# Performance work log

Measured on AMD Instinct MI355X. Metric: run time of the kernel, lower is better.

## Reference

```python
import jax, jax.numpy as jnp
import numpy as np
import math

B = 1; SEQ = 2048; CHUNK = 16; K = SEQ // CHUNK
DIM = 1024; NH = 16; HD = DIM // NH
NL = 2; NLF = 2; HID = 4096; VOCAB = 32000; CSP_MAX = 4
EPS = 1e-5
BS = CHUNK + 2                 # per-chunk decoder block: [fx, sep, tokens]
L = K * BS + 2                 # + trailing [fx_last, sep]


def rope_cache(n_pos, n_elem, base=10000.0):
    theta = 1.0 / (base ** (jnp.arange(0, n_elem, 2, dtype=jnp.float32) / n_elem))
    idx = jnp.outer(jnp.arange(n_pos, dtype=jnp.float32), theta)  # [n_pos, n_elem/2]
    cos = jnp.concatenate([jnp.cos(idx), jnp.cos(idx)], -1)
    sin = jnp.concatenate([jnp.sin(idx), jnp.sin(idx)], -1)
    return cos, sin  # [n_pos, n_elem]


def apply_rope(x, cos, sin):
    # x: [b, h, l, d]; cos/sin: [l, d] (rope_n_elem == head_dim)
    h = x.shape[-1] // 2
    rot = jnp.concatenate([-x[..., h:], x[..., :h]], -1)
    return x * cos + rot * sin


def rmsnorm(x, w):
    return x * jax.lax.rsqrt(jnp.mean(x * x, -1, keepdims=True) + EPS) * w


def attention(x, wqkv, wo, cos, sin, mask):
    b, l, d = x.shape
    qkv = (x @ wqkv).reshape(b, l, 3, NH, HD).transpose(2, 0, 3, 1, 4)
    q, k, v = qkv[0], qkv[1], qkv[2]            # [b, h, l, hd]
    q = apply_rope(q, cos, sin)
    k = apply_rope(k, cos, sin)
    s = jnp.einsum('bhqd,bhkd->bhqk', q, k) / math.sqrt(HD)
    if mask is not None:
        s = jnp.where(mask, s, jnp.float32(-1e30))
    o = jnp.einsum('bhqk,bhkd->bhqd', jax.nn.softmax(s, -1), v)
    return o.transpose(0, 2, 1, 3).reshape(b, l, d) @ wo


def block(x, ln1, wqkv, wo, ln2, wg, wu, wd, cos, sin, mask):
    x = x + attention(rmsnorm(x, ln1), wqkv, wo, cos, sin, mask)
    h = rmsnorm(x, ln2)
    return x + (jax.nn.silu(h @ wg) * (h @ wu)) @ wd


def cat_mask(n, bs):
    # CAT mask: (kv divides block-start | same block) & causal
    q = jnp.arange(n)[:, None]
    kv = jnp.arange(n)[None, :]
    return ((kv % bs == 0) | (q // bs == kv // bs)) & (q >= kv)


def setup_inputs() -> dict:
    key = jax.random.key(0)
    ks = jax.random.split(key, 24)
    w = lambda k, s: jax.random.normal(k, s, jnp.float32) * 0.02
    return {
        'input_ids': jax.random.randint(ks[0], (B, SEQ), 0, VOCAB, dtype=jnp.int32),
        'chunk_size_power': 4,
        'f_wte': w(ks[1], (VOCAB, DIM)), 'f_pos': w(ks[2], (SEQ, DIM)),
        'f_adapt': w(ks[3], (CSP_MAX + 1, DIM)),
        'f_ln1': jnp.ones((NLF, DIM)), 'f_ln2': jnp.ones((NLF, DIM)),
        'f_wqkv': w(ks[4], (NLF, DIM, 3 * DIM)), 'f_wo': w(ks[5], (NLF, DIM, DIM)),
        'f_wg': w(ks[6], (NLF, DIM, HID)), 'f_wu': w(ks[7], (NLF, DIM, HID)),
        'f_wd': w(ks[8], (NLF, HID, DIM)),
        'f_norm': jnp.ones((DIM,)), 'f_proj': w(ks[9], (DIM, CHUNK * DIM)),
        'dummy_fx': w(ks[10], (CSP_MAX + 1, DIM)), 'wte': w(ks[11], (VOCAB, DIM)),
        'sep': w(ks[12], (1, DIM)),
        'd_ln1': jnp.ones((NL, DIM)), 'd_ln2': jnp.ones((NL, DIM)),
        'd_wqkv': w(ks[13], (NL, DIM, 3 * DIM)), 'd_wo': w(ks[14], (NL, DIM, DIM)),
        'd_wg': w(ks[15], (NL, DIM, HID)), 'd_wu': w(ks[16], (NL, DIM, HID)),
        'd_wd': w(ks[17], (NL, HID, DIM)),
        'd_norm': jnp.ones((DIM,)), 'w_out': w(ks[18], (VOCAB, DIM)),
    }


def reference(input_ids, chunk_size_power, f_wte, f_pos, f_adapt, f_ln1, f_ln2,
              f_wqkv, f_wo, f_wg, f_wu, f_wd, f_norm, f_proj, dummy_fx, wte, sep,
              d_ln1, d_ln2, d_wqkv, d_wo, d_wg, d_wu, d_wd, d_norm, w_out):
    csp = int(chunk_size_power)
    ids = input_ids.reshape(B, K, CHUNK)
    cosf, sinf = rope_cache(2 + CHUNK, HD)

    def compress(ids_c, chunk_idx):
        # ids_c: [B, CHUNK] (one chunk, vmapped over K)
        x = f_wte[ids_c]
        adaptive = jnp.broadcast_to(f_adapt[csp], (B, 1, DIM))
        pos_tok = jnp.broadcast_to(f_pos[chunk_idx], (B, 1, DIM))
        x = jnp.concatenate([adaptive, pos_tok, x], 1)  # [B, CHUNK+2, DIM]
        for i in range(NLF):
            x = block(x, f_ln1[i], f_wqkv[i], f_wo[i], f_ln2[i],
                      f_wg[i], f_wu[i], f_wd[i], cosf, sinf, None)
        x = rmsnorm(x, f_norm)[:, 2:, :].reshape(B, CHUNK * DIM)
        # chunk_size_power == log2(CHUNK): bilinear interpolate to same size == identity
        return x @ f_proj.T  # [B, DIM]

    fx = jax.vmap(compress, in_axes=(1, 0), out_axes=1)(ids, jnp.arange(K))  # [B, K, DIM]

    fx_last = fx[:, -1:, :]
    dummy = jnp.broadcast_to(dummy_fx[csp], (B, 1, DIM))
    fx_sh = jnp.concatenate([dummy, fx[:, :-1, :]], 1)[:, :, None, :]  # [B, K, 1, DIM]
    sep_t = jnp.broadcast_to(sep[0], (B, K, 1, DIM))
    emb = wte[ids]  # [B, K, CHUNK, DIM]
    x = jnp.concatenate([fx_sh, sep_t, emb], 2).reshape(B, K * BS, DIM)
    x = jnp.concatenate([x, fx_last, jnp.broadcast_to(sep[0], (B, 1, DIM))], 1)  # [B, L, DIM]

    # per-block repeating RoPE positions (cache built for len BS, tiled)
    pos = jnp.tile(jnp.arange(BS), K + 1)[:L]
    cosb, sinb = rope_cache(BS, HD)
    cosd, sind = cosb[pos], sinb[pos]
    mask = cat_mask(L, BS)

    for i in range(NL):
        x = block(x, d_ln1[i], d_wqkv[i], d_wo[i], d_ln2[i],
                  d_wg[i], d_wu[i], d_wd[i], cosd, sind, mask)
    x = rmsnorm(x, d_norm)
    return x @ w_out.T  # [B, L, VOCAB]
```

## Files before the change

### kernel.cpp

```cpp
#include <hip/hip_runtime.h>
#include <math.h>

#define L_DEC 2306
#define MPAD 2560
#define T_FINE 2304

typedef float f32x4 __attribute__((ext_vector_type(4)));
typedef __bf16 bf16x8 __attribute__((ext_vector_type(8)));
typedef unsigned short u16;
typedef unsigned short us4 __attribute__((ext_vector_type(4)));
typedef unsigned short us8 __attribute__((ext_vector_type(8)));

#define GLOAD16(g, l) __builtin_amdgcn_global_load_lds( \
    (const __attribute__((address_space(1))) unsigned int*)(g), \
    (__attribute__((address_space(3))) unsigned int*)(l), 16, 0, 0)

__device__ __forceinline__ u16 f2bf(float f) {
  unsigned u = __float_as_uint(f);
  u += 0x7fffu + ((u >> 16) & 1u);
  return (u16)(u >> 16);
}

__device__ __forceinline__ int fix_csp(const int* p) {
  int c = p[0];
  if ((unsigned)c <= 4u) return c;
  float f = __uint_as_float((unsigned)c);
  int c2 = (int)f;
  return ((unsigned)c2 <= 4u) ? c2 : 4;
}

__device__ __forceinline__ void xcd_map(int gx, int gy, int& bm, int& bn, int TS) {
  const int nwg = gx * gy;
  const int orig = blockIdx.y * gx + blockIdx.x;
  const int q8 = nwg >> 3, r8 = nwg & 7;
  const int xcd = orig & 7, idx8 = orig >> 3;
  const int wg = (xcd < r8 ? xcd * (q8 + 1) : r8 * (q8 + 1) + (xcd - r8) * q8) + idx8;
  bm = (wg / gx) * TS;
  bn = (wg % gx) * TS;
}

template<int EPI>
__global__ __launch_bounds__(512, 1) void k_gemm3(const u16* __restrict__ A,
                                                  const u16* __restrict__ B,
                                                  float* __restrict__ C,
                                                  int N, int K, int Mstore)
{
  extern __shared__ u16 lds[];
  const int tid = threadIdx.x;
  int bm, bn; xcd_map(gridDim.x, gridDim.y, bm, bn, 256);
  const int w = tid >> 6, lane = tid & 63;
  const int wm = (w >> 2) * 128, wn = (w & 3) * 64;
  const int lr = lane & 15, kh = lane >> 4;

#define STAGE3(buf, kt) do {                                                   \
    u16* lA = lds + (buf) * 32768;                                             \
    u16* lB = lA + 16384;                                                      \
    _Pragma("unroll")                                                          \
    for (int p = 0; p < 4; ++p) {                                              \
      int e = p * 512 + tid;                                                   \
      int row = e >> 3;                                                        \
      int kc = ((e & 7) ^ (row & 7)) * 8;    \
      GLOAD16(A + (size_t)(bm + row) * K + (size_t)(kt) * 64 + kc, lA + e * 8);\
      GLOAD16(B + (size_t)(bn + row) * K + (size_t)(kt) * 64 + kc, lB + e * 8);\
    }                                                                          \
  } while (0)

  f32x4 acc[8][4] = {};
  const int nt = K >> 6;
  STAGE3(0, 0);
  __syncthreads();
  int cur = 0;
  for (int t = 0; t < nt; ++t) {
    if (t + 1 < nt) STAGE3(cur ^ 1, t + 1);
    const u16* pA = lds + cur * 32768;
    const u16* pB = pA + 16384;
    const int xr = (lr & 7) << 3;
#pragma unroll
    for (int kt2 = 0; kt2 < 2; ++kt2) {
      bf16x8 af[8], bf[4];
#pragma unroll
      for (int m = 0; m < 8; ++m)
        af[m] = *(const bf16x8*)&pA[(wm + m * 16 + lr) * 64 + ((kt2 * 32 + kh * 8) ^ xr)];
#pragma unroll
      for (int n = 0; n < 4; ++n)
        bf[n] = *(const bf16x8*)&pB[(wn + n * 16 + lr) * 64 + ((kt2 * 32 + kh * 8) ^ xr)];
#pragma unroll
      for (int m = 0; m < 8; ++m)
#pragma unroll
        for (int n = 0; n < 4; ++n)
          acc[m][n] = __builtin_amdgcn_mfma_f32_16x16x32_bf16(af[m], bf[n], acc[m][n], 0, 0, 0);
    }
    __syncthreads();
    cur ^= 1;
  }
#undef STAGE3

#pragma unroll
  for (int m = 0; m < 8; ++m) {
    int gr0 = bm + wm + m * 16 + kh * 4;
#pragma unroll
    for (int n = 0; n < 4; ++n) {
      int gc = bn + wn + n * 16 + lr;
#pragma unroll
      for (int r = 0; r < 4; ++r) {
        int gr = gr0 + r;
        if (gr < Mstore) C[(size_t)gr * N + gc] = acc[m][n][r];
      }
    }
  }
}

template<int EPI>
__global__ __launch_bounds__(512, 1) void k_gemm2(const u16* __restrict__ A,
                                                  const u16* __restrict__ B,
                                                  float* __restrict__ C,
                                                  u16* __restrict__ Cb,
                                                  int N, int K, int Mstore)
{
  __shared__ u16 As[2][8192];
  __shared__ u16 Bs[2][8192];
  const int tid = threadIdx.x;
  int bm, bn; xcd_map(gridDim.x, gridDim.y, bm, bn, 256);
  const int w = tid >> 6, lane = tid & 63;
  const int wm = (w >> 2) * 128, wn = (w & 3) * 64;
  const int lr = lane & 15, kh = lane >> 4;
  const int r0 = tid >> 2;
  const int ksrc = 8 * ((tid & 3) ^ ((tid >> 3) & 3));
  const u16* ga = A + (size_t)(bm + r0) * K + ksrc;
  const u16* gb = B + (size_t)(bn + r0) * K + ksrc;
  const size_t rstep = (size_t)128 * K;
  const int cola = (kh * 8) ^ (((lr >> 1) & 3) << 3);

#define STAGE2(buf, kt) do {                                   \
    const u16* gA = ga + (size_t)(kt) * 32;                    \
    const u16* gB = gb + (size_t)(kt) * 32;                    \
    GLOAD16(gA,         &As[buf][tid * 8]);                    \
    GLOAD16(gA + rstep, &As[buf][tid * 8 + 4096]);             \
    GLOAD16(gB,         &Bs[buf][tid * 8]);                    \
    GLOAD16(gB + rstep, &Bs[buf][tid * 8 + 4096]);             \
  } while (0)

  f32x4 acc[8][4] = {};
  const int nt = K >> 5;
  STAGE2(0, 0);
  __syncthreads();
  int cur = 0;
  for (int t = 0; t < nt; ++t) {
    if (t + 1 < nt) STAGE2(cur ^ 1, t + 1);
    bf16x8 af[8], bf[4];
#pragma unroll
    for (int m = 0; m < 8; ++m)
      af[m] = *(const bf16x8*)&As[cur][(wm + m * 16 + lr) * 32 + cola];
#pragma unroll
    for (int n = 0; n < 4; ++n)
      bf[n] = *(const bf16x8*)&Bs[cur][(wn + n * 16 + lr) * 32 + cola];
#pragma unroll
    for (int m = 0; m < 8; ++m)
#pragma unroll
      for (int n = 0; n < 4; ++n)
        acc[m][n] = __builtin_amdgcn_mfma_f32_16x16x32_bf16(af[m], bf[n], acc[m][n], 0, 0, 0);
    __syncthreads();
    cur ^= 1;
  }
#undef STAGE2

#pragma unroll
  for (int m = 0; m < 8; ++m) {
    int gr0 = bm + wm + m * 16 + kh * 4;
#pragma unroll
    for (int n = 0; n < 4; ++n) {
      int gc = bn + wn + n * 16 + lr;
#pragma unroll
      for (int r = 0; r < 4; ++r) {
        int gr = gr0 + r;
        if (gr < Mstore) C[(size_t)gr * N + gc] = acc[m][n][r];
      }
    }
  }
}

template<int EPI>
__global__ __launch_bounds__(256) void k_gemm_bt(const u16* __restrict__ A,
                                                 const u16* __restrict__ B,
                                                 float* __restrict__ C,
                                                 u16* __restrict__ Cb,
                                                 int N, int K, int Mstore, int kchunk)
{
  __shared__ u16 As[4096];
  __shared__ u16 Bs[4096];
  const int tid = threadIdx.x;
  int bm, bn; xcd_map(gridDim.x, gridDim.y, bm, bn, 128);
  const int k0 = blockIdx.z * kchunk;
  const int w = tid >> 6, lane = tid & 63;
  const int wm = (w >> 1) * 64, wn = (w & 1) * 64;
  const int lr = lane & 15, kh = lane >> 4;
  const int r0 = tid >> 2;
  const int ksrc = 8 * ((tid & 3) ^ ((tid >> 3) & 3));
  const int cola = (kh * 8) ^ (((lr >> 1) & 3) << 3);

  const u16* ga = A + (size_t)(bm + r0) * K + k0 + ksrc;
  const u16* gb = B + (size_t)(bn + r0) * K + k0 + ksrc;
  u16* la = &As[tid * 8];
  u16* lb = &Bs[tid * 8];
  const size_t rstep = (size_t)64 * K;

  f32x4 acc[4][4] = {};
  for (int kk = 0; kk < kchunk; kk += 32) {
    GLOAD16(ga, la); GLOAD16(ga + rstep, la + 2048);
    GLOAD16(gb, lb); GLOAD16(gb + rstep, lb + 2048);
    ga += 32; gb += 32;
    __syncthreads();
    bf16x8 af[4], bfr[4];
#pragma unroll
    for (int m = 0; m < 4; ++m)
      af[m] = *(const bf16x8*)&As[(wm + m * 16 + lr) * 32 + cola];
#pragma unroll
    for (int n = 0; n < 4; ++n)
      bfr[n] = *(const bf16x8*)&Bs[(wn + n * 16 + lr) * 32 + cola];
#pragma unroll
    for (int m = 0; m < 4; ++m)
#pragma unroll
      for (int n = 0; n < 4; ++n)
        acc[m][n] = __builtin_amdgcn_mfma_f32_16x16x32_bf16(af[m], bfr[n], acc[m][n], 0, 0, 0);
    __syncthreads();
  }

  float* Cz = (EPI == 0) ? C + (size_t)blockIdx.z * Mstore * N : C;
  const int N2 = N >> 1;
#pragma unroll
  for (int m = 0; m < 4; ++m) {
    int gr0 = bm + wm + m * 16 + kh * 4;
#pragma unroll
    for (int n = 0; n < 4; ++n) {
      int gc = bn + wn + n * 16 + lr;
#pragma unroll
      for (int r = 0; r < 4; ++r) {
        int gr = gr0 + r;
        if (EPI == 2) {
          float x = acc[m][n][r];
          float px = __shfl_xor(x, 1);
          if (!(lr & 1) && gr < Mstore) {
            float s = x / (1.f + expf(-x)) * px;
            Cb[(size_t)gr * N2 + (gc >> 1)] = f2bf(s);
          }
        } else if (gr < Mstore) {
          size_t off = (size_t)gr * N + gc;
          if (EPI == 0) Cz[off] = acc[m][n][r];
          else          C[off] += acc[m][n][r];
        }
      }
    }
  }
}

__global__ __launch_bounds__(256) void k_gemm_hf(const u16* __restrict__ A,
                                                 const float* __restrict__ B,
                                                 float* __restrict__ C,
                                                 int N, int K, int Mstore)
{
  __shared__ u16 As[4096];
  __shared__ u16 Bs[4096];
  const int tid = threadIdx.x;
  const int bm = blockIdx.y * 128, bn = blockIdx.x * 128;
  const int w = tid >> 6, lane = tid & 63;
  const int wm = (w >> 1) * 64, wn = (w & 1) * 64;
  const int lr = lane & 15, kh = lane >> 4;
  const int r0 = tid >> 2;
  const int ksrc = 8 * ((tid & 3) ^ ((tid >> 3) & 3));
  const int cola = (kh * 8) ^ (((lr >> 1) & 3) << 3);
  const u16* ga = A + (size_t)(bm + r0) * K + ksrc;
  u16* la = &As[tid * 8];
  const size_t rstep = (size_t)64 * K;

  f32x4 acc[4][4] = {};
  for (int kk = 0; kk < K; kk += 32) {
    GLOAD16(ga, la); GLOAD16(ga + rstep, la + 2048);
    ga += 32;
#pragma unroll
    for (int p = 0; p < 4; ++p) {
      int e = tid + p * 256;
      int row = e >> 3, kc = (e & 7) * 4;
      int kcs = kc ^ (((row >> 1) & 3) << 3);
      float4 v = *(const float4*)(B + (size_t)(bn + row) * K + kk + kc);
      us4 pk; pk[0] = f2bf(v.x); pk[1] = f2bf(v.y); pk[2] = f2bf(v.z); pk[3] = f2bf(v.w);
      *(us4*)&Bs[row * 32 + kcs] = pk;
    }
    __syncthreads();
    bf16x8 af[4], bfr[4];
#pragma unroll
    for (int m = 0; m < 4; ++m)
      af[m] = *(const bf16x8*)&As[(wm + m * 16 + lr) * 32 + cola];
#pragma unroll
    for (int n = 0; n < 4; ++n)
      bfr[n] = *(const bf16x8*)&Bs[(wn + n * 16 + lr) * 32 + cola];
#pragma unroll
    for (int m = 0; m < 4; ++m)
#pragma unroll
      for (int n = 0; n < 4; ++n)
        acc[m][n] = __builtin_amdgcn_mfma_f32_16x16x32_bf16(af[m], bfr[n], acc[m][n], 0, 0, 0);
    __syncthreads();
  }
#pragma unroll
  for (int m = 0; m < 4; ++m) {
    int gr0 = bm + wm + m * 16 + kh * 4;
#pragma unroll
    for (int n = 0; n < 4; ++n) {
      int gc = bn + wn + n * 16 + lr;
#pragma unroll
      for (int r = 0; r < 4; ++r) {
        int gr = gr0 + r;
        if (gr < Mstore) C[(size_t)gr * N + gc] = acc[m][n][r];
      }
    }
  }
}

__global__ __launch_bounds__(256) void k_wt2(const float* __restrict__ W, u16* __restrict__ Wt,
                                             int K, int N, int rs, int ro) {
  __shared__ u16 t[64][80];
  int n0 = blockIdx.x * 64, k0 = blockIdx.y * 64;
#pragma unroll
  for (int p = 0; p < 4; ++p) {
    int id = threadIdx.x + p * 256;
    int row = id >> 4, c4 = (id & 15) * 4;
    float4 v = *(const float4*)(W + (size_t)(k0 + row) * N + n0 + c4);
    t[c4 + 0][row] = f2bf(v.x);
    t[c4 + 1][row] = f2bf(v.y);
    t[c4 + 2][row] = f2bf(v.z);
    t[c4 + 3][row] = f2bf(v.w);
  }
  __syncthreads();
#pragma unroll
  for (int p = 0; p < 2; ++p) {
    int id = threadIdx.x + p * 256;
    int row = id >> 3, c8 = (id & 7) * 8;
    *(us8*)(Wt + ((size_t)(n0 + row) * rs + ro) * K + k0 + c8) = *(const us8*)&t[row][c8];
  }
}

__global__ void k_cvt(const float* __restrict__ x, u16* __restrict__ y, int n4) {
  for (int i = blockIdx.x * 256 + threadIdx.x; i < n4; i += gridDim.x * 256) {
    float4 v = ((const float4*)x)[i];
    us4 p; p[0] = f2bf(v.x); p[1] = f2bf(v.y); p[2] = f2bf(v.z); p[3] = f2bf(v.w);
    ((us4*)y)[i] = p;
  }
}

__global__ void k_reduce_add(const float* __restrict__ p, float* __restrict__ dst,
                             int n, int planes, int addDst) {
  for (int i = blockIdx.x * 256 + threadIdx.x; i < n; i += gridDim.x * 256) {
    float s = addDst ? dst[i] : 0.f;
    for (int z = 0; z < planes; ++z) s += p[(size_t)z * n + i];
    dst[i] = s;
  }
}

__global__ void k_rope_table(float* __restrict__ cosT, float* __restrict__ sinT) {
  int i = blockIdx.x * blockDim.x + threadIdx.x;
  if (i >= 18 * 64) return;
  int p = i >> 6, d = i & 63;
  float theta = powf(10000.f, -(float)(d & 31) / 32.f);
  float ang = (float)p * theta;
  cosT[i] = cosf(ang);
  sinT[i] = sinf(ang);
}

__global__ void k_fine_embed(const int* __restrict__ ids, const int* __restrict__ cspp,
                             const float* __restrict__ f_wte, const float* __restrict__ f_pos,
                             const float* __restrict__ f_adapt, float* __restrict__ xF) {
  int csp = fix_csp(cspp);
  for (int idx = blockIdx.x * 256 + threadIdx.x; idx < T_FINE * 1024; idx += gridDim.x * 256) {
    int r = idx >> 10, d = idx & 1023;
    int c = r / 18, j = r - c * 18;
    float v;
    if (j == 0)      v = f_adapt[csp * 1024 + d];
    else if (j == 1) v = f_pos[c * 1024 + d];
    else             v = f_wte[(size_t)ids[c * 16 + j - 2] * 1024 + d];
    xF[idx] = v;
  }
}

__global__ __launch_bounds__(256) void k_rmsnorm_bf(const float* __restrict__ x,
                                                    const float* __restrict__ w,
                                                    u16* __restrict__ y) {
  int t = blockIdx.x;
  const float4 v = *(const float4*)(x + (size_t)t * 1024 + threadIdx.x * 4);
  float ss = v.x * v.x + v.y * v.y + v.z * v.z + v.w * v.w;
#pragma unroll
  for (int off = 32; off; off >>= 1) ss += __shfl_xor(ss, off);
  __shared__ float ps[4];
  if ((threadIdx.x & 63) == 0) ps[threadIdx.x >> 6] = ss;
  __syncthreads();
  float inv = rsqrtf((ps[0] + ps[1] + ps[2] + ps[3]) * (1.f / 1024.f) + 1e-5f);
  const float4 wv = *(const float4*)(w + threadIdx.x * 4);
  us4 o;
  o[0] = f2bf(v.x * inv * wv.x); o[1] = f2bf(v.y * inv * wv.y);
  o[2] = f2bf(v.z * inv * wv.z); o[3] = f2bf(v.w * inv * wv.w);
  *(us4*)(y + (size_t)t * 1024 + threadIdx.x * 4) = o;
}

__global__ __launch_bounds__(256) void k_rmsnorm_pack_bf(const float* __restrict__ x,
                                                         const float* __restrict__ w,
                                                         u16* __restrict__ y) {
  int b = blockIdx.x;
  int c = b >> 4, r = b & 15;
  const float* xr = x + (size_t)(c * 18 + 2 + r) * 1024;
  const float4 v = *(const float4*)(xr + threadIdx.x * 4);
  float ss = v.x * v.x + v.y * v.y + v.z * v.z + v.w * v.w;
#pragma unroll
  for (int off = 32; off; off >>= 1) ss += __shfl_xor(ss, off);
  __shared__ float ps[4];
  if ((threadIdx.x & 63) == 0) ps[threadIdx.x >> 6] = ss;
  __syncthreads();
  float inv = rsqrtf((ps[0] + ps[1] + ps[2] + ps[3]) * (1.f / 1024.f) + 1e-5f);
  const float4 wv = *(const float4*)(w + threadIdx.x * 4);
  us4 o;
  o[0] = f2bf(v.x * inv * wv.x); o[1] = f2bf(v.y * inv * wv.y);
  o[2] = f2bf(v.z * inv * wv.z); o[3] = f2bf(v.w * inv * wv.w);
  *(us4*)(y + (size_t)b * 1024 + threadIdx.x * 4) = o;
}

__global__ __launch_bounds__(256) void k_rope(float* __restrict__ qkv,
                                              const float* __restrict__ cosT,
                                              const float* __restrict__ sinT) {
  int t = blockIdx.x;
  int p = t % 18;
  float* row = qkv + (size_t)t * 3072;
#pragma unroll
  for (int i = 0; i < 4; ++i) {
    int it = threadIdx.x + i * 256;
    int s = it >> 9, rem = it & 511, h = rem >> 5, d = rem & 31;
    float* px = row + s * 1024 + h * 64 + d;
    float x1 = px[0], x2 = px[32];
    float cv = cosT[p * 64 + d], sv = sinT[p * 64 + d];
    px[0]  = x1 * cv - x2 * sv;
    px[32] = x2 * cv + x1 * sv;
  }
}

__global__ __launch_bounds__(256) void k_attn_fine2(const float* __restrict__ qkv,
                                                    u16* __restrict__ out) {
  __shared__ float q[4][18][68], k[4][18][68], v[4][18][68], s[4][18][20];
  int c = blockIdx.x;
  int w = threadIdx.x >> 6, lane = threadIdx.x & 63;
  int h = blockIdx.y * 4 + w;
  const float* base = qkv + (size_t)c * 18 * 3072 + h * 64;
#pragma unroll 3
  for (int r = 0; r < 18; ++r) {
    q[w][r][lane] = base[(size_t)r * 3072 + lane];
    k[w][r][lane] = base[(size_t)r * 3072 + 1024 + lane];
    v[w][r][lane] = base[(size_t)r * 3072 + 2048 + lane];
  }
  __syncthreads();
#pragma unroll
  for (int it = 0; it < 6; ++it) {
    int idx = lane + it * 64;
    if (idx < 324) {
      int qi = (idx * 3641) >> 16;
      int ki = idx - qi * 18;
      const float* qr = q[w][qi];
      const float* kr = k[w][ki];
      float a = 0.f;
#pragma unroll
      for (int d = 0; d < 64; d += 4) {
        float4 x = *(const float4*)&qr[d];
        float4 y = *(const float4*)&kr[d];
        a += x.x * y.x + x.y * y.y + x.z * y.z + x.w * y.w;
      }
      s[w][qi][ki] = a * 0.125f;
    }
  }
  __syncthreads();
  if (lane < 18) {
    float mx = -1e30f;
#pragma unroll
    for (int j = 0; j < 18; ++j) mx = fmaxf(mx, s[w][lane][j]);
    float sum = 0.f;
#pragma unroll
    for (int j = 0; j < 18; ++j) { float e = expf(s[w][lane][j] - mx); s[w][lane][j] = e; sum += e; }
    float inv = 1.f / sum;
#pragma unroll
    for (int j = 0; j < 18; ++j) s[w][lane][j] *= inv;
  }
  __syncthreads();
  float vcol[18];
#pragma unroll
  for (int ki = 0; ki < 18; ++ki) vcol[ki] = v[w][ki][lane];
#pragma unroll 2
  for (int qi = 0; qi < 18; ++qi) {
    float o = 0.f;
#pragma unroll
    for (int ki = 0; ki < 18; ++ki) o += s[w][qi][ki] * vcol[ki];
    out[(size_t)(c * 18 + qi) * 1024 + h * 64 + lane] = f2bf(o);
  }
}

__global__ __launch_bounds__(256) void k_attn_dec2(const float* __restrict__ qkv,
                                                   u16* __restrict__ out) {
  __shared__ float sc_s[4][160];
  int t = blockIdx.x;
  int w = threadIdx.x >> 6, lane = threadIdx.x & 63;
  int h = blockIdx.y * 4 + w;
  float* sc = sc_s[w];
  int bq = t / 18;
  int nstart = bq + 1;
  int nown = t - 18 * bq;
  int nk = nstart + nown;
  int g = lane >> 2, j = lane & 3;
  const float* qb = qkv + (size_t)t * 3072 + h * 64 + j * 16;
  float4 q0 = *(const float4*)(qb);
  float4 q1 = *(const float4*)(qb + 4);
  float4 q2 = *(const float4*)(qb + 8);
  float4 q3 = *(const float4*)(qb + 12);
  for (int i0 = 0; i0 < nk; i0 += 16) {
    int i = i0 + g;
    float p = 0.f;
    if (i < nk) {
      int kv = (i < nstart) ? 18 * i : 18 * bq + (i - nstart) + 1;
      const float* kp = qkv + (size_t)kv * 3072 + 1024 + h * 64 + j * 16;
      float4 k0 = *(const float4*)(kp);
      float4 k1 = *(const float4*)(kp + 4);
      float4 k2 = *(const float4*)(kp + 8);
      float4 k3 = *(const float4*)(kp + 12);
      p = q0.x * k0.x + q0.y * k0.y + q0.z * k0.z + q0.w * k0.w
        + q1.x * k1.x + q1.y * k1.y + q1.z * k1.z + q1.w * k1.w
        + q2.x * k2.x + q2.y * k2.y + q2.z * k2.z + q2.w * k2.w
        + q3.x * k3.x + q3.y * k3.y + q3.z * k3.z + q3.w * k3.w;
    }
    p += __shfl_xor(p, 1);
    p += __shfl_xor(p, 2);
    if (i < nk && j == 0) sc[i] = p * 0.125f;
  }
  __syncthreads();
  float mx = -1e30f;
  for (int i = lane; i < nk; i += 64) mx = fmaxf(mx, sc[i]);
#pragma unroll
  for (int off = 32; off; off >>= 1) mx = fmaxf(mx, __shfl_xor(mx, off));
  float sum = 0.f;
  for (int i = lane; i < nk; i += 64) { float e = expf(sc[i] - mx); sc[i] = e; sum += e; }
#pragma unroll
  for (int off = 32; off; off >>= 1) sum += __shfl_xor(sum, off);
  float inv = 1.f / sum;
  __syncthreads();
  const float* vb = qkv + 2048 + h * 64 + lane;
  float o0 = 0.f, o1 = 0.f, o2 = 0.f, o3 = 0.f;
  int i = 0;
  for (; i + 4 <= nk; i += 4) {
    int ia = i, ib = i + 1, ic = i + 2, id = i + 3;
    int kva = (ia < nstart) ? 18 * ia : 18 * bq + (ia - nstart) + 1;
    int kvb = (ib < nstart) ? 18 * ib : 18 * bq + (ib - nstart) + 1;
    int kvc = (ic < nstart) ? 18 * ic : 18 * bq + (ic - nstart) + 1;
    int kvd = (id < nstart) ? 18 * id : 18 * bq + (id - nstart) + 1;
    o0 += sc[ia] * vb[(size_t)kva * 3072];
    o1 += sc[ib] * vb[(size_t)kvb * 3072];
    o2 += sc[ic] * vb[(size_t)kvc * 3072];
    o3 += sc[id] * vb[(size_t)kvd * 3072];
  }
  for (; i < nk; ++i) {
    int kv = (i < nstart) ? 18 * i : 18 * bq + (i - nstart) + 1;
    o0 += sc[i] * vb[(size_t)kv * 3072];
  }
  float o = (o0 + o1) + (o2 + o3);
  out[(size_t)t * 1024 + h * 64 + lane] = f2bf(o * inv);
}

__global__ void k_assemble(const int* __restrict__ ids, const int* __restrict__ cspp,
                           const float* __restrict__ fx, const float* __restrict__ dummy_fx,
                           const float* __restrict__ sep, const float* __restrict__ wte,
                           float* __restrict__ xD) {
  int csp = fix_csp(cspp);
  for (int idx = blockIdx.x * 256 + threadIdx.x; idx < MPAD * 1024; idx += gridDim.x * 256) {
    int t = idx >> 10, d = idx & 1023;
    float v;
    if (t >= L_DEC)     v = 0.f;
    else if (t == 2305) v = sep[d];
    else if (t == 2304) v = fx[127 * 1024 + d];
    else {
      int k = t / 18, r = t - k * 18;
      if (r == 0)      v = (k == 0) ? dummy_fx[csp * 1024 + d] : fx[(k - 1) * 1024 + d];
      else if (r == 1) v = sep[d];
      else             v = wte[(size_t)ids[k * 16 + r - 2] * 1024 + d];
    }
    xD[idx] = v;
  }
}

extern "C" void kernel_launch(void* const* d_in, const int* in_sizes, int n_in,
                              void* d_out, int out_size, void* d_ws, size_t ws_size,
                              hipStream_t stream) {
  const int*   input_ids = (const int*)d_in[0];
  const int*   cspp      = (const int*)d_in[1];
  const float* f_wte     = (const float*)d_in[2];
  const float* f_pos     = (const float*)d_in[3];
  const float* f_adapt   = (const float*)d_in[4];
  const float* f_ln1     = (const float*)d_in[5];
  const float* f_ln2     = (const float*)d_in[6];
  const float* f_wqkv    = (const float*)d_in[7];
  const float* f_wo      = (const float*)d_in[8];
  const float* f_wg      = (const float*)d_in[9];
  const float* f_wu      = (const float*)d_in[10];
  const float* f_wd      = (const float*)d_in[11];
  const float* f_norm    = (const float*)d_in[12];
  const float* f_proj    = (const float*)d_in[13];
  const float* dummy_fx  = (const float*)d_in[14];
  const float* wte       = (const float*)d_in[15];
  const float* sep       = (const float*)d_in[16];
  const float* d_ln1     = (const float*)d_in[17];
  const float* d_ln2     = (const float*)d_in[18];
  const float* d_wqkv    = (const float*)d_in[19];
  const float* d_wo      = (const float*)d_in[20];
  const float* d_wg      = (const float*)d_in[21];
  const float* d_wu      = (const float*)d_in[22];
  const float* d_wd      = (const float*)d_in[23];
  const float* d_norm    = (const float*)d_in[24];
  const float* w_out     = (const float*)d_in[25];

  float* cosT = (float*)d_ws;
  float* sinT = cosT + 1152;
  u16*   bufH = (u16*)(sinT + 1152);
  u16*   w_outb = bufH + (size_t)MPAD * 1024;
  const size_t WS_NEED = 2 * 1152 * 4 + (size_t)MPAD * 1024 * 2 + (size_t)32000 * 1024 * 2;
  const bool big_ws = ws_size >= WS_NEED;

  float* o       = (float*)d_out;
  float* xF      = o;
  float* xD      = xF + (size_t)T_FINE * 1024;
  float* fx      = xD + (size_t)MPAD * 1024;
  float* bufQKV  = fx + 128 * 1024;
  u16*   bufA    = (u16*)(bufQKV + (size_t)MPAD * 3072);
  u16*   bufGb   = bufA + (size_t)MPAD * 1024;
  u16*   packedb = bufGb + (size_t)MPAD * 4096;
  u16*   Wt      = packedb + (size_t)128 * 16384;
  u16*   projb   = Wt + (size_t)8192 * 1024;
  float* spk     = (float*)(projb + (size_t)1024 * 16384);

#define GEMM_BT(EPI, Ap, Bp, Cp, Cbp, Mpad, N, K, Mstore, S) \
  k_gemm_bt<EPI><<<dim3((N) / 128, (Mpad) / 128, (S)), 256, 0, stream>>>((Ap), (Bp), (Cp), (Cbp), (N), (K), (Mstore), (K) / (S))

  k_rope_table<<<5, 256, 0, stream>>>(cosT, sinT);
  k_fine_embed<<<2048, 256, 0, stream>>>(input_ids, cspp, f_wte, f_pos, f_adapt, xF);

  for (int i = 0; i < 2; ++i) {
    k_rmsnorm_bf<<<T_FINE, 256, 0, stream>>>(xF, f_ln1 + i * 1024, bufH);
    k_wt2<<<dim3(48, 16), 256, 0, stream>>>(f_wqkv + (size_t)i * 1024 * 3072, Wt, 1024, 3072, 1, 0);
    GEMM_BT(0, bufH, Wt, bufQKV, (u16*)nullptr, T_FINE, 3072, 1024, T_FINE, 1);
    k_rope<<<T_FINE, 256, 0, stream>>>(bufQKV, cosT, sinT);
    k_attn_fine2<<<dim3(128, 4), 256, 0, stream>>>(bufQKV, bufA);
    k_wt2<<<dim3(16, 16), 256, 0, stream>>>(f_wo + (size_t)i * 1024 * 1024, Wt, 1024, 1024, 1, 0);
    GEMM_BT(1, bufA, Wt, xF, (u16*)nullptr, T_FINE, 1024, 1024, T_FINE, 1);
    k_rmsnorm_bf<<<T_FINE, 256, 0, stream>>>(xF, f_ln2 + i * 1024, bufH);
    k_wt2<<<dim3(64, 16), 256, 0, stream>>>(f_wg + (size_t)i * 1024 * 4096, Wt, 1024, 4096, 2, 0);
    k_wt2<<<dim3(64, 16), 256, 0, stream>>>(f_wu + (size_t)i * 1024 * 4096, Wt, 1024, 4096, 2, 1);
    GEMM_BT(2, bufH, Wt, (float*)nullptr, bufGb, T_FINE, 8192, 1024, T_FINE, 1);
    k_wt2<<<dim3(16, 64), 256, 0, stream>>>(f_wd + (size_t)i * 4096 * 1024, Wt, 4096, 1024, 1, 0);
    GEMM_BT(0, bufGb, Wt, spk, (u16*)nullptr, T_FINE, 1024, 4096, T_FINE, 4);
    k_reduce_add<<<2048, 256, 0, stream>>>(spk, xF, T_FINE * 1024, 4, 1);
  }

  k_rmsnorm_pack_bf<<<2048, 256, 0, stream>>>(xF, f_norm, packedb);
  k_cvt<<<2048, 256, 0, stream>>>(f_proj, projb, 1024 * 16384 / 4);
  GEMM_BT(0, packedb, projb, spk, (u16*)nullptr, 128, 1024, 16384, 128, 32);
  k_reduce_add<<<512, 256, 0, stream>>>(spk, fx, 128 * 1024, 32, 0);

  k_assemble<<<2048, 256, 0, stream>>>(input_ids, cspp, fx, dummy_fx, sep, wte, xD);
  for (int i = 0; i < 2; ++i) {
    k_rmsnorm_bf<<<MPAD, 256, 0, stream>>>(xD, d_ln1 + i * 1024, bufH);
    k_wt2<<<dim3(48, 16), 256, 0, stream>>>(d_wqkv + (size_t)i * 1024 * 3072, Wt, 1024, 3072, 1, 0);
    GEMM_BT(0, bufH, Wt, bufQKV, (u16*)nullptr, MPAD, 3072, 1024, MPAD, 1);
    k_rope<<<L_DEC, 256, 0, stream>>>(bufQKV, cosT, sinT);
    k_attn_dec2<<<dim3(L_DEC, 4), 256, 0, stream>>>(bufQKV, bufA);
    k_wt2<<<dim3(16, 16), 256, 0, stream>>>(d_wo + (size_t)i * 1024 * 1024, Wt, 1024, 1024, 1, 0);
    GEMM_BT(1, bufA, Wt, xD, (u16*)nullptr, MPAD, 1024, 1024, MPAD, 1);
    k_rmsnorm_bf<<<MPAD, 256, 0, stream>>>(xD, d_ln2 + i * 1024, bufH);
    k_wt2<<<dim3(64, 16), 256, 0, stream>>>(d_wg + (size_t)i * 1024 * 4096, Wt, 1024, 4096, 2, 0);
    k_wt2<<<dim3(64, 16), 256, 0, stream>>>(d_wu + (size_t)i * 1024 * 4096, Wt, 1024, 4096, 2, 1);
    GEMM_BT(2, bufH, Wt, (float*)nullptr, bufGb, MPAD, 8192, 1024, MPAD, 1);
    k_wt2<<<dim3(16, 64), 256, 0, stream>>>(d_wd + (size_t)i * 4096 * 1024, Wt, 4096, 1024, 1, 0);
    GEMM_BT(0, bufGb, Wt, spk, (u16*)nullptr, MPAD, 1024, 4096, MPAD, 4);
    k_reduce_add<<<2048, 256, 0, stream>>>(spk, xD, MPAD * 1024, 4, 1);
  }

  k_rmsnorm_bf<<<MPAD, 256, 0, stream>>>(xD, d_norm, bufH);
  if (big_ws) {
    k_cvt<<<2048, 256, 0, stream>>>(w_out, w_outb, 32000 * 1024 / 4);
    hipError_t ae = hipFuncSetAttribute(
        reinterpret_cast<const void*>(&k_gemm3<0>),
        hipFuncAttributeMaxDynamicSharedMemorySize, 131072);
    if (ae == hipSuccess) {
      k_gemm3<0><<<dim3(125, 10), 512, 131072, stream>>>(bufH, w_outb, o, 32000, 1024, L_DEC);
    } else {
      k_gemm2<0><<<dim3(125, 10), 512, 0, stream>>>(bufH, w_outb, o, nullptr, 32000, 1024, L_DEC);
    }
  } else {
    k_gemm_hf<<<dim3(250, MPAD / 128), 256, 0, stream>>>(bufH, w_out, o, 32000, 1024, L_DEC);
  }
#undef GEMM_BT
}
```

Before: 1.489 ms.

## Stage per-block K/V in LDS for decoder CAT attention, one block per chunk-head

Replaces the per-query decoder attention kernel with one workgroup per (chunk, head) that loads the shared block-start keys and the chunk's own keys and values into LDS once. All 18 queries of the chunk reuse them, so K/V are no longer re-read from global memory for every query. The grid becomes 129x16 with 512 threads and roughly 80 KB of dynamic LDS, which reduces parallelism and occupancy. Late chunks that stage about 146 rows get more work than early ones, which adds load imbalance. The old kernel remains as a fallback if the LDS attribute call fails.

```diff
diff --git a/kernel.cpp b/kernel.cpp
--- a/kernel.cpp
+++ b/kernel.cpp
@@ -492,6 +492,76 @@
 #pragma unroll
     for (int ki = 0; ki < 18; ++ki) o += s[w][qi][ki] * vcol[ki];
     out[(size_t)(c * 18 + qi) * 1024 + h * 64 + lane] = f2bf(o);
+  }
+}
+
+__global__ __launch_bounds__(512) void k_attn_dec3(const float* __restrict__ qkv,
+                                                   u16* __restrict__ out) {
+  extern __shared__ float dyn[];
+  float* Kl = dyn;
+  float* Vl = Kl + 146 * 65;
+  float* Ql = Vl + 146 * 65;
+  float* Sw = Ql + 18 * 65;
+  const int bq = blockIdx.x, h = blockIdx.y;
+  const int w = threadIdx.x >> 6, lane = threadIdx.x & 63;
+  const int t0 = 18 * bq;
+  const int nq = (bq < 128) ? 18 : 2;
+  const int nstage = (bq < 128) ? (bq + 18) : 130;
+
+  {
+    int rr = threadIdx.x >> 2, c = threadIdx.x & 3;
+    for (int row = rr; row < nstage; row += 128) {
+      int kv = (row <= bq) ? 18 * row : t0 + (row - bq);
+      const float* kp = qkv + (size_t)kv * 3072 + 1024 + h * 64 + c * 16;
+#pragma unroll
+      for (int q4 = 0; q4 < 4; ++q4) {
+        float4 a = *(const float4*)(kp + q4 * 4);
+        float4 b = *(const float4*)(kp + 1024 + q4 * 4);
+        int d = c * 16 + q4 * 4;
+        float* kd = Kl + row * 65 + d;
+        float* vd = Vl + row * 65 + d;
+        kd[0] = a.x; kd[1] = a.y; kd[2] = a.z; kd[3] = a.w;
+        vd[0] = b.x; vd[1] = b.y; vd[2] = b.z; vd[3] = b.w;
+      }
+    }
+    if (rr < nq) {
+      const float* qp = qkv + (size_t)(t0 + rr) * 3072 + h * 64 + c * 16;
+#pragma unroll
+      for (int q4 = 0; q4 < 4; ++q4) {
+        float4 a = *(const float4*)(qp + q4 * 4);
+        int d = c * 16 + q4 * 4;
+        float* qd = Ql + rr * 65 + d;
+        qd[0] = a.x; qd[1] = a.y; qd[2] = a.z; qd[3] = a.w;
+      }
+    }
+  }
+  __syncthreads();
+
+  for (int r = w; r < nq; r += 8) {
+    const int nk = bq + 1 + r;
+    float* S = Sw + w * 148;
+    const float* qr = Ql + r * 65;
+    float mx = -1e30f;
+    for (int i = lane; i < nk; i += 64) {
+      const float* kr = Kl + i * 65;
+      float a = 0.f;
+#pragma unroll
+      for (int d = 0; d < 64; ++d) a += qr[d] * kr[d];
+      a *= 0.125f;
+      S[i] = a;
+      mx = fmaxf(mx, a);
+    }
+#pragma unroll
+    for (int off = 32; off; off >>= 1) mx = fmaxf(mx, __shfl_xor(mx, off));
+    float sum = 0.f;
+    for (int i = lane; i < nk; i += 64) { float e = expf(S[i] - mx); S[i] = e; sum += e; }
+#pragma unroll
+    for (int off = 32; off; off >>= 1) sum += __shfl_xor(sum, off);
+    float inv = 1.f / sum;
+    __builtin_amdgcn_wave_barrier();
+    float o = 0.f;
+    for (int i = 0; i < nk; ++i) o += S[i] * Vl[i * 65 + lane];
+    out[(size_t)(t0 + r) * 1024 + h * 64 + lane] = f2bf(o * inv);
   }
 }
 
@@ -634,6 +704,11 @@
   u16*   projb   = Wt + (size_t)8192 * 1024;
   float* spk     = (float*)(projb + (size_t)1024 * 16384);
 
+  const size_t ATTN_LDS = (size_t)(146 * 65 * 2 + 18 * 65 + 8 * 148) * 4;
+  hipError_t eattn = hipFuncSetAttribute(
+      reinterpret_cast<const void*>(&k_attn_dec3),
+      hipFuncAttributeMaxDynamicSharedMemorySize, (int)ATTN_LDS);
+
 #define GEMM_BT(EPI, Ap, Bp, Cp, Cbp, Mpad, N, K, Mstore, S) \
   k_gemm_bt<EPI><<<dim3((N) / 128, (Mpad) / 128, (S)), 256, 0, stream>>>((Ap), (Bp), (Cp), (Cbp), (N), (K), (Mstore), (K) / (S))
 
@@ -668,7 +743,11 @@
     k_wt2<<<dim3(48, 16), 256, 0, stream>>>(d_wqkv + (size_t)i * 1024 * 3072, Wt, 1024, 3072, 1, 0);
     GEMM_BT(0, bufH, Wt, bufQKV, (u16*)nullptr, MPAD, 3072, 1024, MPAD, 1);
     k_rope<<<L_DEC, 256, 0, stream>>>(bufQKV, cosT, sinT);
-    k_attn_dec2<<<dim3(L_DEC, 4), 256, 0, stream>>>(bufQKV, bufA);
+    if (eattn == hipSuccess) {
+      k_attn_dec3<<<dim3(129, 16), 512, ATTN_LDS, stream>>>(bufQKV, bufA);
+    } else {
+      k_attn_dec2<<<dim3(L_DEC, 4), 256, 0, stream>>>(bufQKV, bufA);
+    }
     k_wt2<<<dim3(16, 16), 256, 0, stream>>>(d_wo + (size_t)i * 1024 * 1024, Wt, 1024, 1024, 1, 0);
     GEMM_BT(1, bufA, Wt, xD, (u16*)nullptr, MPAD, 1024, 1024, MPAD, 1);
     k_rmsnorm_bf<<<MPAD, 256, 0, stream>>>(xD, d_ln2 + i * 1024, bufH);
```

Measured after the change: 1.504 ms. Within noise of the previous version (+1.0%).
